# Optimization experiments

Hardware: AMD Instinct MI355X
Metric: run time of the kernel (lower is better)

## Reference

```python
import jax, jax.numpy as jnp
import numpy as np

H, F, E = 256, 512, 8  # hidden_dim, ffn_dim, num_experts


def setup_inputs() -> dict:
    key = jax.random.key(0)
    ks = jax.random.split(key, 7)
    B, S = 8, 4096
    s = lambda fan_in: 1.0 / np.sqrt(fan_in)
    x = jax.random.normal(ks[0], (B, S, H), dtype=jnp.float32)
    Wg = jax.random.uniform(ks[1], (H, E), jnp.float32, -s(H), s(H))
    bg = jnp.zeros((E,), jnp.float32)
    W1 = jax.random.uniform(ks[2], (E, H, F), jnp.float32, -s(H), s(H))
    b1 = jax.random.uniform(ks[3], (E, F), jnp.float32, -s(H), s(H))
    W2 = jax.random.uniform(ks[4], (E, F, H), jnp.float32, -s(F), s(F))
    b2 = jax.random.uniform(ks[5], (E, H), jnp.float32, -s(F), s(F))
    return {"x": x, "Wg": Wg, "bg": bg, "W1": W1, "b1": b1, "W2": W2, "b2": b2}


def reference(x, Wg, bg, W1, b1, W2, b2):
    # gate probabilities over experts: [B,S,E]
    gate_probs = jax.nn.softmax(x @ Wg + bg, axis=-1)
    # all-expert FFN (dense MoE): batched GEMMs over the expert axis
    h = jnp.einsum('bsh,ehf->ebsf', x, W1) + b1[:, None, None, :]   # [E,B,S,F]
    h = jax.nn.gelu(h, approximate=False)                            # torch nn.GELU (erf)
    y = jnp.einsum('ebsf,efh->ebsh', h, W2) + b2[:, None, None, :]  # [E,B,S,H]
    # gate-weighted sum over experts
    mixed = jnp.einsum('ebsh,bse->bsh', y, gate_probs)               # [B,S,H]
    return mixed  # dropout=0.0 / eval mode -> identity
```

## Files before the change

kernel.cpp:

```cpp
#include <hip/hip_runtime.h>
#include <hip/hip_bf16.h>
#include <math.h>

#define H 256
#define F 512
#define E 8
#define T_TOK 32768
#define BM 128
#define FC 64
#define NCH 64

typedef float    f32x4 __attribute__((__ext_vector_type__(4)));
typedef _Float16 f16x8 __attribute__((__ext_vector_type__(8)));
typedef _Float16 f16x4 __attribute__((__ext_vector_type__(4)));

#define BAR_LG()  asm volatile("s_waitcnt lgkmcnt(0)\ns_barrier" ::: "memory")
#define BAR_ALL() asm volatile("s_waitcnt vmcnt(0) lgkmcnt(0)\ns_barrier" ::: "memory")

__device__ __forceinline__ void async_copy16(const void* g, void* l) {
    __builtin_amdgcn_global_load_lds((const __attribute__((address_space(1))) void*)g,
                                     (__attribute__((address_space(3))) void*)l, 16, 0, 0);
}

__device__ __forceinline__ float gelu_fast(float v) {
    const float c1 = 2.302117236f;
    const float c2 = 0.102943842f;
    float u2 = v * fmaf(c2, v * v, c1);
    float ex = __builtin_amdgcn_exp2f(u2);
    float r = __builtin_amdgcn_rcpf(ex + 1.0f);
    return v - v * r;
}

__global__ void prep_w1(const float* __restrict__ in, _Float16* __restrict__ out) {
    __shared__ float t[32][33];
    int e = blockIdx.z, f0 = blockIdx.x * 32, h0 = blockIdx.y * 32;
    int tx = threadIdx.x, ty = threadIdx.y;
    const float* ip = in + ((size_t)e * H + h0) * F + f0;
    for (int i = 0; i < 32; i += 8) t[ty + i][tx] = ip[(size_t)(ty + i) * F + tx];
    __syncthreads();
    _Float16* op = out + (size_t)e * F * H;
    for (int i = 0; i < 32; i += 8) {
        int f = f0 + ty + i, h = h0 + tx;
        op[(size_t)f * H + (h ^ ((f & 7) << 3))] = (_Float16)t[tx][ty + i];
    }
}

__global__ void prep_w2(const float* __restrict__ in, _Float16* __restrict__ out) {
    __shared__ float t[32][33];
    int e = blockIdx.z, h0 = blockIdx.x * 32, f0 = blockIdx.y * 32;
    int tx = threadIdx.x, ty = threadIdx.y;
    const float* ip = in + ((size_t)e * F + f0) * H + h0;
    for (int i = 0; i < 32; i += 8) t[ty + i][tx] = ip[(size_t)(ty + i) * H + tx];
    __syncthreads();
    _Float16* op = out + (size_t)e * 8 * 256 * 64;
    for (int i = 0; i < 32; i += 8) {
        int h = h0 + ty + i, f = f0 + tx;
        op[((size_t)(f >> 6) * 256 + h) * 64 + ((f & 63) ^ ((h & 7) << 3))] = (_Float16)t[tx][ty + i];
    }
}

__global__ void gate_kernel(const float* __restrict__ x, const float* __restrict__ Wg,
                            const float* __restrict__ bg, float* __restrict__ probs) {
    int gid = blockIdx.x * blockDim.x + threadIdx.x;
    int t = gid >> 3, e = gid & 7;
    const float* xr = x + (size_t)t * H;
    float acc = 0.f;
    for (int k = 0; k < H; k += 4) {
        float4 xv = *(const float4*)(xr + k);
        acc += xv.x * Wg[(k + 0) * E + e] + xv.y * Wg[(k + 1) * E + e]
             + xv.z * Wg[(k + 2) * E + e] + xv.w * Wg[(k + 3) * E + e];
    }
    acc += bg[e];
    float m = acc;
    for (int s = 1; s < 8; s <<= 1) m = fmaxf(m, __shfl_xor(m, s, 8));
    float p = expf(acc - m);
    float sum = p;
    for (int s = 1; s < 8; s <<= 1) sum += __shfl_xor(sum, s, 8);
    probs[gid] = p / sum;
}

__device__ __forceinline__ void stage_chunk(const _Float16* W1t, const _Float16* W2t,
                                            int s, _Float16* w1d, _Float16* w2d,
                                            int wid, int lane) {
    const char* w1src = (const char*)W1t + (size_t)s * 32768;
    const char* w2src = (const char*)W2t + (size_t)s * 32768;
#pragma unroll
    for (int q = 0; q < 4; ++q) {
        int o = (wid * 4 + q) * 1024 + lane * 16;
        async_copy16(w1src + o, (char*)w1d + o);
        async_copy16(w2src + o, (char*)w2d + o);
    }
}

__global__ __launch_bounds__(512, 2) void moe_main(
    const float* __restrict__ x, const _Float16* __restrict__ W1t,
    const float* __restrict__ b1, const _Float16* __restrict__ W2t,
    const float* __restrict__ b2, const float* __restrict__ probs,
    float* __restrict__ out) {

    __shared__ __align__(16) _Float16 w1s[2][FC * H];
    __shared__ __align__(16) _Float16 w2s[2][H * FC];
    __shared__ __align__(16) _Float16 hs[BM * FC];

    int tid = threadIdx.x;
    int lane = tid & 63, wid = tid >> 6;
    int t0 = blockIdx.x * BM;
    int l15 = lane & 15, l4 = lane >> 4;

    int fw = wid >> 2, tw1 = wid & 3;
    int hw = wid >> 1, tw2 = wid & 1;

    f16x8 xf[8][2];
#pragma unroll
    for (int j = 0; j < 2; ++j) {
        const float* xr = x + (size_t)(t0 + tw1 * 32 + j * 16 + l15) * H + (l4 << 3);
#pragma unroll
        for (int ks = 0; ks < 8; ++ks) {
            float4 v0 = *(const float4*)(xr + ks * 32);
            float4 v1 = *(const float4*)(xr + ks * 32 + 4);
            f16x8 hv;
            hv[0] = (_Float16)v0.x; hv[1] = (_Float16)v0.y; hv[2] = (_Float16)v0.z; hv[3] = (_Float16)v0.w;
            hv[4] = (_Float16)v1.x; hv[5] = (_Float16)v1.y; hv[6] = (_Float16)v1.z; hv[7] = (_Float16)v1.w;
            xf[ks][j] = hv;
        }
    }

    stage_chunk(W1t, W2t, 0, w1s[0], w2s[0], wid, lane);
    BAR_ALL();

    f32x4 yacc[4][4];
#pragma unroll
    for (int i = 0; i < 4; ++i)
#pragma unroll
        for (int j = 0; j < 4; ++j) yacc[i][j] = (f32x4){0.f, 0.f, 0.f, 0.f};

    for (int e = 0; e < E; ++e) {
        float pg0 = probs[(size_t)(t0 + tw1 * 32 + l15) * E + e];
        float pg1 = probs[(size_t)(t0 + tw1 * 32 + 16 + l15) * E + e];

        for (int c = 0; c < F / FC; ++c) {
            int s = e * 8 + c;
            int b = s & 1;
            int fbase = c * FC;
            const _Float16* w1p = w1s[b];
            const _Float16* w2p = w2s[b];

            if (s + 1 < NCH)
                stage_chunk(W1t, W2t, s + 1, w1s[b ^ 1], w2s[b ^ 1], wid, lane);

            f32x4 hacc[2][2];
            hacc[0][0] = hacc[0][1] = hacc[1][0] = hacc[1][1] = (f32x4){0.f, 0.f, 0.f, 0.f};
            __builtin_amdgcn_s_setprio(1);
#pragma unroll
            for (int ks = 0; ks < 8; ++ks) {
                int kidx = ks * 32 + (l4 << 3);
                int fr0 = fw * 32 + l15, fr1 = fr0 + 16;
                f16x8 a0 = *(const f16x8*)&w1p[fr0 * H + (kidx ^ ((fr0 & 7) << 3))];
                f16x8 a1 = *(const f16x8*)&w1p[fr1 * H + (kidx ^ ((fr1 & 7) << 3))];
                hacc[0][0] = __builtin_amdgcn_mfma_f32_16x16x32_f16(a0, xf[ks][0], hacc[0][0], 0, 0, 0);
                hacc[0][1] = __builtin_amdgcn_mfma_f32_16x16x32_f16(a0, xf[ks][1], hacc[0][1], 0, 0, 0);
                hacc[1][0] = __builtin_amdgcn_mfma_f32_16x16x32_f16(a1, xf[ks][0], hacc[1][0], 0, 0, 0);
                hacc[1][1] = __builtin_amdgcn_mfma_f32_16x16x32_f16(a1, xf[ks][1], hacc[1][1], 0, 0, 0);
            }
            __builtin_amdgcn_s_setprio(0);

            f16x8 av[4][2];
#pragma unroll
            for (int i = 0; i < 4; ++i) {
                int hr = hw * 64 + i * 16 + l15;
                int base = hr * FC;
                int sw = (hr & 7) << 3;
                av[i][0] = *(const f16x8*)&w2p[base + (((l4 << 3)) ^ sw)];
                av[i][1] = *(const f16x8*)&w2p[base + ((32 + (l4 << 3)) ^ sw)];
            }
#pragma unroll
            for (int i = 0; i < 2; ++i) {
                int flocal = (fw * 2 + i) * 16 + l4 * 4;
                float4 bv = *(const float4*)(b1 + (size_t)e * F + fbase + flocal);
#pragma unroll
                for (int j = 0; j < 2; ++j) {
                    int tokl = tw1 * 32 + j * 16 + l15;
                    float p = j ? pg1 : pg0;
                    f32x4 hv = hacc[i][j];
                    f16x4 hp;
                    hp[0] = (_Float16)(p * gelu_fast(hv[0] + bv.x));
                    hp[1] = (_Float16)(p * gelu_fast(hv[1] + bv.y));
                    hp[2] = (_Float16)(p * gelu_fast(hv[2] + bv.z));
                    hp[3] = (_Float16)(p * gelu_fast(hv[3] + bv.w));
                    int idx = (tokl * FC + flocal) ^ ((tokl & 7) << 3);
                    *(f16x4*)&hs[idx] = hp;
                }
            }
            BAR_LG();

            __builtin_amdgcn_s_setprio(1);
#pragma unroll
            for (int ks = 0; ks < FC / 32; ++ks) {
                int kidx = ks * 32 + (l4 << 3);
                f16x8 bv2[4];
#pragma unroll
                for (int j = 0; j < 4; ++j) {
                    int tok = tw2 * 64 + j * 16 + l15;
                    bv2[j] = *(const f16x8*)&hs[(tok * FC + kidx) ^ ((tok & 7) << 3)];
                }
#pragma unroll
                for (int i = 0; i < 4; ++i)
#pragma unroll
                    for (int j = 0; j < 4; ++j)
                        yacc[i][j] = __builtin_amdgcn_mfma_f32_16x16x32_f16(av[i][ks], bv2[j], yacc[i][j], 0, 0, 0);
            }
            __builtin_amdgcn_s_setprio(0);
            BAR_ALL();
        }
    }

#pragma unroll
    for (int j = 0; j < 4; ++j) {
        int tok = t0 + tw2 * 64 + j * 16 + l15;
        float pe[8];
#pragma unroll
        for (int e = 0; e < 8; ++e) pe[e] = probs[(size_t)tok * E + e];
#pragma unroll
        for (int i = 0; i < 4; ++i) {
            int h0 = hw * 64 + i * 16 + l4 * 4;
            f32x4 acc = yacc[i][j];
#pragma unroll
            for (int e = 0; e < 8; ++e) {
                float4 b2v = *(const float4*)(b2 + (size_t)e * H + h0);
                acc[0] += pe[e] * b2v.x;
                acc[1] += pe[e] * b2v.y;
                acc[2] += pe[e] * b2v.z;
                acc[3] += pe[e] * b2v.w;
            }
            *(f32x4*)(out + (size_t)tok * H + h0) = acc;
        }
    }
}

extern "C" void kernel_launch(void* const* d_in, const int* in_sizes, int n_in,
                              void* d_out, int out_size, void* d_ws, size_t ws_size,
                              hipStream_t stream) {
    const float* x  = (const float*)d_in[0];
    const float* Wg = (const float*)d_in[1];
    const float* bg = (const float*)d_in[2];
    const float* W1 = (const float*)d_in[3];
    const float* b1 = (const float*)d_in[4];
    const float* W2 = (const float*)d_in[5];
    const float* b2 = (const float*)d_in[6];
    float* out = (float*)d_out;

    _Float16* W1t = (_Float16*)d_ws;
    _Float16* W2t = W1t + (size_t)E * F * H;
    float* probs  = (float*)(W2t + (size_t)E * H * F);

    dim3 tb(32, 8);
    prep_w1<<<dim3(F / 32, H / 32, E), tb, 0, stream>>>(W1, W1t);
    prep_w2<<<dim3(H / 32, F / 32, E), tb, 0, stream>>>(W2, W2t);
    gate_kernel<<<(T_TOK * E) / 256, 256, 0, stream>>>(x, Wg, bg, probs);
    moe_main<<<T_TOK / BM, 512, 0, stream>>>(x, W1t, b1, W2t, b2, probs, out);
}
```

Before: 226.0 us.

## Halve token tile, load pre-packed W2 fragments directly to registers, double-buffer hidden

```diff
diff --git a/kernel.cpp b/kernel.cpp
--- a/kernel.cpp
+++ b/kernel.cpp
@@ -6,7 +6,7 @@
 #define F 512
 #define E 8
 #define T_TOK 32768
-#define BM 128
+#define BM 64
 #define FC 64
 #define NCH 64
 
@@ -14,7 +14,6 @@
 typedef _Float16 f16x8 __attribute__((__ext_vector_type__(8)));
 typedef _Float16 f16x4 __attribute__((__ext_vector_type__(4)));
 
-#define BAR_LG()  asm volatile("s_waitcnt lgkmcnt(0)\ns_barrier" ::: "memory")
 #define BAR_ALL() asm volatile("s_waitcnt vmcnt(0) lgkmcnt(0)\ns_barrier" ::: "memory")
 
 __device__ __forceinline__ void async_copy16(const void* g, void* l) {
@@ -45,17 +44,33 @@
     }
 }
 
-__global__ void prep_w2(const float* __restrict__ in, _Float16* __restrict__ out) {
-    __shared__ float t[32][33];
-    int e = blockIdx.z, h0 = blockIdx.x * 32, f0 = blockIdx.y * 32;
-    int tx = threadIdx.x, ty = threadIdx.y;
-    const float* ip = in + ((size_t)e * F + f0) * H + h0;
-    for (int i = 0; i < 32; i += 8) t[ty + i][tx] = ip[(size_t)(ty + i) * H + tx];
+__global__ void prep_w2p(const float* __restrict__ in, _Float16* __restrict__ out) {
+    __shared__ float t[64][65];
+    int blk = blockIdx.x;
+    int s = blk >> 2, hw = blk & 3;
+    int e = s >> 3, c = s & 7;
+    int tid = threadIdx.x;
+    int fl = tid >> 2, h16 = (tid & 3) * 16;
+    const float* ip = in + ((size_t)(e * F + c * 64 + fl)) * H + hw * 64 + h16;
+#pragma unroll
+    for (int q = 0; q < 4; ++q) {
+        float4 v = *(const float4*)(ip + q * 4);
+        t[fl][h16 + q * 4 + 0] = v.x;
+        t[fl][h16 + q * 4 + 1] = v.y;
+        t[fl][h16 + q * 4 + 2] = v.z;
+        t[fl][h16 + q * 4 + 3] = v.w;
+    }
     __syncthreads();
-    _Float16* op = out + (size_t)e * 8 * 256 * 64;
-    for (int i = 0; i < 32; i += 8) {
-        int h = h0 + ty + i, f = f0 + tx;
-        op[((size_t)(f >> 6) * 256 + h) * 64 + ((f & 63) ^ ((h & 7) << 3))] = (_Float16)t[tx][ty + i];
+#pragma unroll
+    for (int r = 0; r < 2; ++r) {
+        int g = tid * 2 + r;
+        int lane = g & 63, iks = g >> 6;
+        int fb = (iks & 1) * 32 + (lane >> 4) * 8;
+        int hl = (iks >> 1) * 16 + (lane & 15);
+        f16x8 v;
+#pragma unroll
+        for (int d = 0; d < 8; ++d) v[d] = (_Float16)t[fb + d][hl];
+        *(f16x8*)(out + (size_t)s * 16384 + ((size_t)hw * 512 + g) * 8) = v;
     }
 }
 
@@ -79,28 +94,24 @@
     probs[gid] = p / sum;
 }
 
-__device__ __forceinline__ void stage_chunk(const _Float16* W1t, const _Float16* W2t,
-                                            int s, _Float16* w1d, _Float16* w2d,
-                                            int wid, int lane) {
-    const char* w1src = (const char*)W1t + (size_t)s * 32768;
-    const char* w2src = (const char*)W2t + (size_t)s * 32768;
+__device__ __forceinline__ void stage_w1(const _Float16* W1t, int s, _Float16* w1d,
+                                         int wid, int lane) {
+    const char* src = (const char*)W1t + (size_t)s * 32768;
 #pragma unroll
     for (int q = 0; q < 4; ++q) {
         int o = (wid * 4 + q) * 1024 + lane * 16;
-        async_copy16(w1src + o, (char*)w1d + o);
-        async_copy16(w2src + o, (char*)w2d + o);
-    }
-}
-
-__global__ __launch_bounds__(512, 2) void moe_main(
+        async_copy16(src + o, (char*)w1d + o);
+    }
+}
+
+__global__ __launch_bounds__(512, 4) void moe_main(
     const float* __restrict__ x, const _Float16* __restrict__ W1t,
-    const float* __restrict__ b1, const _Float16* __restrict__ W2t,
+    const float* __restrict__ b1, const _Float16* __restrict__ W2p,
     const float* __restrict__ b2, const float* __restrict__ probs,
     float* __restrict__ out) {
 
     __shared__ __align__(16) _Float16 w1s[2][FC * H];
-    __shared__ __align__(16) _Float16 w2s[2][H * FC];
-    __shared__ __align__(16) _Float16 hs[BM * FC];
+    __shared__ __align__(16) _Float16 hs[2][BM * FC];
 
     int tid = threadIdx.x;
     int lane = tid & 63, wid = tid >> 6;
@@ -110,10 +121,9 @@
     int fw = wid >> 2, tw1 = wid & 3;
     int hw = wid >> 1, tw2 = wid & 1;
 
-    f16x8 xf[8][2];
-#pragma unroll
-    for (int j = 0; j < 2; ++j) {
-        const float* xr = x + (size_t)(t0 + tw1 * 32 + j * 16 + l15) * H + (l4 << 3);
+    f16x8 xf[8];
+    {
+        const float* xr = x + (size_t)(t0 + tw1 * 16 + l15) * H + (l4 << 3);
 #pragma unroll
         for (int ks = 0; ks < 8; ++ks) {
             float4 v0 = *(const float4*)(xr + ks * 32);
@@ -121,102 +131,97 @@
             f16x8 hv;
             hv[0] = (_Float16)v0.x; hv[1] = (_Float16)v0.y; hv[2] = (_Float16)v0.z; hv[3] = (_Float16)v0.w;
             hv[4] = (_Float16)v1.x; hv[5] = (_Float16)v1.y; hv[6] = (_Float16)v1.z; hv[7] = (_Float16)v1.w;
-            xf[ks][j] = hv;
-        }
-    }
-
-    stage_chunk(W1t, W2t, 0, w1s[0], w2s[0], wid, lane);
+            xf[ks] = hv;
+        }
+    }
+    float pg[8];
+    {
+        const float* pp = probs + (size_t)(t0 + tw1 * 16 + l15) * E;
+        float4 p0 = *(const float4*)pp, p1 = *(const float4*)(pp + 4);
+        pg[0] = p0.x; pg[1] = p0.y; pg[2] = p0.z; pg[3] = p0.w;
+        pg[4] = p1.x; pg[5] = p1.y; pg[6] = p1.z; pg[7] = p1.w;
+    }
+
+    stage_w1(W1t, 0, w1s[0], wid, lane);
     BAR_ALL();
 
-    f32x4 yacc[4][4];
+    f32x4 yacc[4][2];
 #pragma unroll
     for (int i = 0; i < 4; ++i)
 #pragma unroll
-        for (int j = 0; j < 4; ++j) yacc[i][j] = (f32x4){0.f, 0.f, 0.f, 0.f};
-
-    for (int e = 0; e < E; ++e) {
-        float pg0 = probs[(size_t)(t0 + tw1 * 32 + l15) * E + e];
-        float pg1 = probs[(size_t)(t0 + tw1 * 32 + 16 + l15) * E + e];
-
-        for (int c = 0; c < F / FC; ++c) {
-            int s = e * 8 + c;
-            int b = s & 1;
-            int fbase = c * FC;
-            const _Float16* w1p = w1s[b];
-            const _Float16* w2p = w2s[b];
-
-            if (s + 1 < NCH)
-                stage_chunk(W1t, W2t, s + 1, w1s[b ^ 1], w2s[b ^ 1], wid, lane);
-
-            f32x4 hacc[2][2];
-            hacc[0][0] = hacc[0][1] = hacc[1][0] = hacc[1][1] = (f32x4){0.f, 0.f, 0.f, 0.f};
-            __builtin_amdgcn_s_setprio(1);
-#pragma unroll
-            for (int ks = 0; ks < 8; ++ks) {
-                int kidx = ks * 32 + (l4 << 3);
-                int fr0 = fw * 32 + l15, fr1 = fr0 + 16;
-                f16x8 a0 = *(const f16x8*)&w1p[fr0 * H + (kidx ^ ((fr0 & 7) << 3))];
-                f16x8 a1 = *(const f16x8*)&w1p[fr1 * H + (kidx ^ ((fr1 & 7) << 3))];
-                hacc[0][0] = __builtin_amdgcn_mfma_f32_16x16x32_f16(a0, xf[ks][0], hacc[0][0], 0, 0, 0);
-                hacc[0][1] = __builtin_amdgcn_mfma_f32_16x16x32_f16(a0, xf[ks][1], hacc[0][1], 0, 0, 0);
-                hacc[1][0] = __builtin_amdgcn_mfma_f32_16x16x32_f16(a1, xf[ks][0], hacc[1][0], 0, 0, 0);
-                hacc[1][1] = __builtin_amdgcn_mfma_f32_16x16x32_f16(a1, xf[ks][1], hacc[1][1], 0, 0, 0);
+        for (int j = 0; j < 2; ++j) yacc[i][j] = (f32x4){0.f, 0.f, 0.f, 0.f};
+
+    for (int s = 0; s < NCH; ++s) {
+        int b = s & 1;
+        int e = s >> 3, c = s & 7, fbase = c * FC;
+        const _Float16* w1p = w1s[b];
+
+        f16x8 av[4][2];
+        {
+            const _Float16* wb = W2p + (size_t)s * 16384 + ((size_t)(hw * 8) * 64 + lane) * 8;
+#pragma unroll
+            for (int i = 0; i < 4; ++i) {
+                av[i][0] = *(const f16x8*)(wb + (i * 2 + 0) * 512);
+                av[i][1] = *(const f16x8*)(wb + (i * 2 + 1) * 512);
             }
-            __builtin_amdgcn_s_setprio(0);
-
-            f16x8 av[4][2];
-#pragma unroll
-            for (int i = 0; i < 4; ++i) {
-                int hr = hw * 64 + i * 16 + l15;
-                int base = hr * FC;
-                int sw = (hr & 7) << 3;
-                av[i][0] = *(const f16x8*)&w2p[base + (((l4 << 3)) ^ sw)];
-                av[i][1] = *(const f16x8*)&w2p[base + ((32 + (l4 << 3)) ^ sw)];
+        }
+        float4 bvq[2];
+#pragma unroll
+        for (int i = 0; i < 2; ++i)
+            bvq[i] = *(const float4*)(b1 + (size_t)e * F + fbase + (fw * 2 + i) * 16 + l4 * 4);
+
+        if (s + 1 < NCH)
+            stage_w1(W1t, s + 1, w1s[b ^ 1], wid, lane);
+
+        f32x4 hacc[2];
+        hacc[0] = hacc[1] = (f32x4){0.f, 0.f, 0.f, 0.f};
+#pragma unroll
+        for (int ks = 0; ks < 8; ++ks) {
+            int kidx = ks * 32 + (l4 << 3);
+            int fr0 = fw * 32 + l15, fr1 = fr0 + 16;
+            f16x8 a0 = *(const f16x8*)&w1p[fr0 * H + (kidx ^ ((fr0 & 7) << 3))];
+            f16x8 a1 = *(const f16x8*)&w1p[fr1 * H + (kidx ^ ((fr1 & 7) << 3))];
+            hacc[0] = __builtin_amdgcn_mfma_f32_16x16x32_f16(a0, xf[ks], hacc[0], 0, 0, 0);
+            hacc[1] = __builtin_amdgcn_mfma_f32_16x16x32_f16(a1, xf[ks], hacc[1], 0, 0, 0);
+        }
+
+        float p = pg[e];
+#pragma unroll
+        for (int i = 0; i < 2; ++i) {
+            int flocal = (fw * 2 + i) * 16 + l4 * 4;
+            float4 bv = bvq[i];
+            int tokl = tw1 * 16 + l15;
+            f16x4 hp;
+            hp[0] = (_Float16)(p * gelu_fast(hacc[i][0] + bv.x));
+            hp[1] = (_Float16)(p * gelu_fast(hacc[i][1] + bv.y));
+            hp[2] = (_Float16)(p * gelu_fast(hacc[i][2] + bv.z));
+            hp[3] = (_Float16)(p * gelu_fast(hacc[i][3] + bv.w));
+            int idx = (tokl * FC + flocal) ^ ((tokl & 7) << 3);
+            *(f16x4*)&hs[b][idx] = hp;
+        }
+        BAR_ALL();
+
+#pragma unroll
+        for (int ks = 0; ks < FC / 32; ++ks) {
+            int kidx = ks * 32 + (l4 << 3);
+            f16x8 bv2[2];
+#pragma unroll
+            for (int j = 0; j < 2; ++j) {
+                int tok = tw2 * 32 + j * 16 + l15;
+                bv2[j] = *(const f16x8*)&hs[b][(tok * FC + kidx) ^ ((tok & 7) << 3)];
             }
 #pragma unroll
-            for (int i = 0; i < 2; ++i) {
-                int flocal = (fw * 2 + i) * 16 + l4 * 4;
-                float4 bv = *(const float4*)(b1 + (size_t)e * F + fbase + flocal);
-#pragma unroll
-                for (int j = 0; j < 2; ++j) {
-                    int tokl = tw1 * 32 + j * 16 + l15;
-                    float p = j ? pg1 : pg0;
-                    f32x4 hv = hacc[i][j];
-                    f16x4 hp;
-                    hp[0] = (_Float16)(p * gelu_fast(hv[0] + bv.x));
-                    hp[1] = (_Float16)(p * gelu_fast(hv[1] + bv.y));
-                    hp[2] = (_Float16)(p * gelu_fast(hv[2] + bv.z));
-                    hp[3] = (_Float16)(p * gelu_fast(hv[3] + bv.w));
-                    int idx = (tokl * FC + flocal) ^ ((tokl & 7) << 3);
-                    *(f16x4*)&hs[idx] = hp;
-                }
-            }
-            BAR_LG();
-
-            __builtin_amdgcn_s_setprio(1);
-#pragma unroll
-            for (int ks = 0; ks < FC / 32; ++ks) {
-                int kidx = ks * 32 + (l4 << 3);
-                f16x8 bv2[4];
-#pragma unroll
-                for (int j = 0; j < 4; ++j) {
-                    int tok = tw2 * 64 + j * 16 + l15;
-                    bv2[j] = *(const f16x8*)&hs[(tok * FC + kidx) ^ ((tok & 7) << 3)];
-                }
-#pragma unroll
-                for (int i = 0; i < 4; ++i)
-#pragma unroll
-                    for (int j = 0; j < 4; ++j)
-                        yacc[i][j] = __builtin_amdgcn_mfma_f32_16x16x32_f16(av[i][ks], bv2[j], yacc[i][j], 0, 0, 0);
-            }
-            __builtin_amdgcn_s_setprio(0);
-            BAR_ALL();
-        }
-    }
-
-#pragma unroll
-    for (int j = 0; j < 4; ++j) {
-        int tok = t0 + tw2 * 64 + j * 16 + l15;
+            for (int i = 0; i < 4; ++i)
+#pragma unroll
+                for (int j = 0; j < 2; ++j)
+                    yacc[i][j] = __builtin_amdgcn_mfma_f32_16x16x32_f16(av[i][ks], bv2[j], yacc[i][j], 0, 0, 0);
+        }
+        BAR_ALL();
+    }
+
+#pragma unroll
+    for (int j = 0; j < 2; ++j) {
+        int tok = t0 + tw2 * 32 + j * 16 + l15;
         float pe[8];
 #pragma unroll
         for (int e = 0; e < 8; ++e) pe[e] = probs[(size_t)tok * E + e];
@@ -250,12 +255,12 @@
     float* out = (float*)d_out;
 
     _Float16* W1t = (_Float16*)d_ws;
-    _Float16* W2t = W1t + (size_t)E * F * H;
-    float* probs  = (float*)(W2t + (size_t)E * H * F);
+    _Float16* W2p = W1t + (size_t)E * F * H;
+    float* probs  = (float*)(W2p + (size_t)64 * 16384);
 
     dim3 tb(32, 8);
     prep_w1<<<dim3(F / 32, H / 32, E), tb, 0, stream>>>(W1, W1t);
-    prep_w2<<<dim3(H / 32, F / 32, E), tb, 0, stream>>>(W2, W2t);
+    prep_w2p<<<256, 256, 0, stream>>>(W2, W2p);
     gate_kernel<<<(T_TOK * E) / 256, 256, 0, stream>>>(x, Wg, bg, probs);
-    moe_main<<<T_TOK / BM, 512, 0, stream>>>(x, W1t, b1, W2t, b2, probs, out);
-}
+    moe_main<<<T_TOK / BM, 512, 0, stream>>>(x, W1t, b1, W2p, b2, probs, out);
+}
```

New measurement: 262.0 us. +15.9%, slower.
